# Performance work log

Hardware: AMD Instinct MI355X
Metric: run time of the kernel (lower is better)

The kernel has to match this reference:

```python
import jax, jax.numpy as jnp
import numpy as np

N, D, H = 512, 512, 1024  # n tokens, per-token dim, hidden; input_dim = 2*D


def setup_inputs() -> dict:
    key = jax.random.key(0)
    k1, k2, k3, k4, k5 = jax.random.split(key, 5)
    inp = jax.random.normal(k1, (N, D), dtype=jnp.float32)
    # torch nn.Linear stores weight [out, in]; we store transposed [in, out]
    s1 = 1.0 / np.sqrt(2 * D)
    W1 = jax.random.uniform(k2, (2 * D, H), dtype=jnp.float32, minval=-s1, maxval=s1)
    b1 = jax.random.uniform(k3, (H,), dtype=jnp.float32, minval=-s1, maxval=s1)
    s2 = 1.0 / np.sqrt(H)
    W2 = jax.random.uniform(k4, (H, 1), dtype=jnp.float32, minval=-s2, maxval=s2)
    b2 = jax.random.uniform(k5, (1,), dtype=jnp.float32, minval=-s2, maxval=s2)
    return {"input": inp, "W1": W1, "b1": b1, "W2": W2, "b2": b2}


def reference(input, W1, b1, W2, b2):
    x = jnp.squeeze(input)                       # [n, d]
    d = x.shape[1]
    # cat(x[i], x[j]) @ W1 == x[i] @ W1[:d] + x[j] @ W1[d:]
    hi = x @ W1[:d]                              # [n, h]
    hj = x @ W1[d:]                              # [n, h]
    h = jnp.tanh(hi[:, None, :] + hj[None, :, :] + b1)  # [n, n, h]
    scores = h @ W2 + b2                         # [n, n, 1]
    return scores[..., 0]                        # [n, n]
```

## Files before the change

### kernel.cpp

```cpp
#include <hip/hip_runtime.h>
#include <math.h>

#define NN 512
#define DD 512
#define HH 1024
#define C2LOG2E 2.8853900817779268f

typedef __attribute__((ext_vector_type(8))) short bf16x8;
typedef __attribute__((ext_vector_type(4))) float f32x4;

static __device__ __forceinline__ float rcp_fast(float x) {
    return __builtin_amdgcn_rcpf(x);
}
static __device__ __forceinline__ float exp2_fast(float x) {
    return __builtin_amdgcn_exp2f(x);
}
static __device__ __forceinline__ ushort f2bf(float f) {
    unsigned u = __float_as_uint(f);
    u += 0x7FFF + ((u >> 16) & 1);
    return (ushort)(u >> 16);
}
static __device__ __forceinline__ float bf2f(short u) {
    return __uint_as_float(((unsigned)(ushort)u) << 16);
}

__global__ __launch_bounds__(256) void k_convert(const float* __restrict__ x,
                                                 const float* __restrict__ W1,
                                                 const float* __restrict__ b2,
                                                 short* __restrict__ xbs,
                                                 short* __restrict__ Bts,
                                                 float* __restrict__ out) {
    __shared__ float ts[64][65];
    const int t = threadIdx.x;
    const int bx = blockIdx.x;
    if (bx < 128) {
        const int q = bx * 256 + t;
        const int g = q >> 10, ktc = (q >> 6) & 15, l = q & 63;
        const int i = g * 16 + (l & 15);
        const int k0 = ktc * 32 + (l >> 4) * 8;
        const float4 v0 = *(const float4*)&x[i * DD + k0];
        const float4 v1 = *(const float4*)&x[i * DD + k0 + 4];
        bf16x8 o;
        o[0] = (short)f2bf(v0.x); o[1] = (short)f2bf(v0.y);
        o[2] = (short)f2bf(v0.z); o[3] = (short)f2bf(v0.w);
        o[4] = (short)f2bf(v1.x); o[5] = (short)f2bf(v1.y);
        o[6] = (short)f2bf(v1.z); o[7] = (short)f2bf(v1.w);
        *(bf16x8*)&xbs[q * 8] = o;
        return;
    }
    if (bx >= 384) {
        const int f4 = (bx - 384) * 256 + t;
        const float b = b2[0];
        float4 o; o.x = b; o.y = b; o.z = b; o.w = b;
        ((float4*)out)[f4] = o;
        return;
    }
    const int tid = bx - 128;
    const int k0 = (tid >> 5) * 64;
    const int nglob = (tid & 31) * 64;
    const int off = (nglob >= 1024) ? 512 : 0;
    const int nm = nglob & 1023;
#pragma unroll
    for (int u = 0; u < 4; ++u) {
        const int f4 = t + u * 256;
        const int r = f4 >> 4, c = (f4 & 15) * 4;
        *(float4*)&ts[r][c] = *(const float4*)&W1[(off + k0 + r) * HH + nm + c];
    }
    __syncthreads();
#pragma unroll
    for (int u = 0; u < 2; ++u) {
        const int q = u * 256 + t;
        const int lg = q >> 7, lc = (q >> 6) & 1, l = q & 63;
        const int n_loc = lg * 16 + (l & 15);
        const int k_loc = lc * 32 + (l >> 4) * 8;
        bf16x8 o;
#pragma unroll
        for (int j = 0; j < 8; ++j) o[j] = (short)f2bf(ts[k_loc + j][n_loc]);
        const int gg = (nglob >> 4) + lg;
        const int ktc = (k0 >> 5) + lc;
        *(bf16x8*)&Bts[((gg * 16 + ktc) * 64 + l) * 8] = o;
    }
}

__global__ __launch_bounds__(256) void k_gemm_mfma(const short* __restrict__ xbs,
                                                   const short* __restrict__ Bts,
                                                   const float* __restrict__ b1,
                                                   short* __restrict__ Ebf) {
    const int t = threadIdx.x;
    const int w = t >> 6, l = t & 63;
    const int gi = blockIdx.x * 4 + w;
    const int by = blockIdx.y;
    const int gn0 = by * 2;

    f32x4 acc[2] = {};
    const short* ap  = xbs + gi * 8192 + l * 8;
    const short* bp0 = Bts + (gn0 + 0) * 8192 + l * 8;
    const short* bp1 = Bts + (gn0 + 1) * 8192 + l * 8;
#pragma unroll
    for (int ktc = 0; ktc < 16; ++ktc) {
        const bf16x8 a = *(const bf16x8*)(ap + ktc * 512);
        acc[0] = __builtin_amdgcn_mfma_f32_16x16x32_bf16(a, *(const bf16x8*)(bp0 + ktc * 512), acc[0], 0, 0, 0);
        acc[1] = __builtin_amdgcn_mfma_f32_16x16x32_bf16(a, *(const bf16x8*)(bp1 + ktc * 512), acc[1], 0, 0, 0);
    }
    const int lm = l & 15;
    const int orow = gi * 16 + (l >> 4) * 4;
    const bool second = (by >= 32);
#pragma unroll
    for (int c = 0; c < 2; ++c) {
        const int n = by * 32 + c * 16 + lm;
        const float badd = second ? b1[n - HH] : 0.0f;
#pragma unroll
        for (int r = 0; r < 4; ++r) {
            Ebf[(orow + r) * (2 * HH) + n] =
                (short)f2bf(exp2_fast(C2LOG2E * (acc[c][r] + badd)));
        }
    }
}

__global__ __launch_bounds__(256) void k_score(const short* __restrict__ Ebf,
                                               const float* __restrict__ W2,
                                               float* __restrict__ out) {
    __shared__ short e1s[64][72];
    __shared__ short e2s[32][72];
    __shared__ float w2s[64];
    const int t = threadIdx.x;
    const int i0 = blockIdx.x * 64, j0 = blockIdx.y * 32;
    const int hb = blockIdx.z * 64;
    const int tx = t & 15, ty = t >> 4;

#pragma unroll
    for (int u = 0; u < 2; ++u) {
        const int q = u * 256 + t;
        const int r = q >> 3, c8 = (q & 7) * 8;
        *(bf16x8*)&e1s[r][c8] = *(const bf16x8*)&Ebf[(i0 + r) * (2 * HH) + hb + c8];
    }
    {
        const int r = t >> 3, c8 = (t & 7) * 8;
        *(bf16x8*)&e2s[r][c8] = *(const bf16x8*)&Ebf[(j0 + r) * (2 * HH) + HH + hb + c8];
    }
    if (t < 64) w2s[t] = W2[hb + t];
    __syncthreads();

    float acc[4][2] = {};
    float sw = 0.0f;
    const int ty4 = ty * 4;
#pragma unroll 2
    for (int s = 0; s < 8; ++s) {
        const int h8 = s * 8;
        float ef[4][8], ff[2][8];
#pragma unroll
        for (int m = 0; m < 4; ++m) {
            const bf16x8 v = *(const bf16x8*)&e1s[ty4 + m][h8];
#pragma unroll
            for (int j = 0; j < 8; ++j) ef[m][j] = bf2f(v[j]);
        }
#pragma unroll
        for (int n = 0; n < 2; ++n) {
            const bf16x8 v = *(const bf16x8*)&e2s[tx + n * 16][h8];
#pragma unroll
            for (int j = 0; j < 8; ++j) ff[n][j] = bf2f(v[j]);
        }
        const float4 wl = *(const float4*)&w2s[h8];
        const float4 wh = *(const float4*)&w2s[h8 + 4];
#pragma unroll
        for (int m = 0; m < 4; ++m) {
#pragma unroll
            for (int n = 0; n < 2; ++n) {
                const float* em = ef[m];
                const float* fn = ff[n];
                const float d0 = __builtin_fmaf(em[0], fn[0], 1.0f);
                const float d1 = __builtin_fmaf(em[1], fn[1], 1.0f);
                const float d2 = __builtin_fmaf(em[2], fn[2], 1.0f);
                const float d3 = __builtin_fmaf(em[3], fn[3], 1.0f);
                const float d4 = __builtin_fmaf(em[4], fn[4], 1.0f);
                const float d5 = __builtin_fmaf(em[5], fn[5], 1.0f);
                const float d6 = __builtin_fmaf(em[6], fn[6], 1.0f);
                const float d7 = __builtin_fmaf(em[7], fn[7], 1.0f);
                const float d01 = d0 * d1, d23 = d2 * d3;
                const float d45 = d4 * d5, d67 = d6 * d7;
                const float n01 = __builtin_fmaf(wl.x, d1, wl.y * d0);
                const float n23 = __builtin_fmaf(wl.z, d3, wl.w * d2);
                const float n45 = __builtin_fmaf(wh.x, d5, wh.y * d4);
                const float n67 = __builtin_fmaf(wh.z, d7, wh.w * d6);
                const float N1 = __builtin_fmaf(n01, d23, n23 * d01);
                const float N2 = __builtin_fmaf(n45, d67, n67 * d45);
                const float D1 = d01 * d23, D2 = d45 * d67;
                const float Nn = __builtin_fmaf(N1, D2, N2 * D1);
                const float Dd = D1 * D2;
                acc[m][n] = __builtin_fmaf(Nn, rcp_fast(Dd), acc[m][n]);
            }
        }
        sw += wl.x + wl.y + wl.z + wl.w + wh.x + wh.y + wh.z + wh.w;
    }

#pragma unroll
    for (int m = 0; m < 4; ++m) {
        const int row = i0 + ty4 + m;
#pragma unroll
        for (int n = 0; n < 2; ++n) {
            const int col = j0 + tx + n * 16;
            atomicAdd(&out[row * NN + col], sw - 2.0f * acc[m][n]);
        }
    }
}

extern "C" void kernel_launch(void* const* d_in, const int* in_sizes, int n_in,
                              void* d_out, int out_size, void* d_ws, size_t ws_size,
                              hipStream_t stream) {
    const float* x  = (const float*)d_in[0];
    const float* W1 = (const float*)d_in[1];
    const float* b1 = (const float*)d_in[2];
    const float* W2 = (const float*)d_in[3];
    const float* b2 = (const float*)d_in[4];
    float* out = (float*)d_out;

    short* Ebf = (short*)d_ws;
    short* xbs = Ebf + NN * 2 * HH;
    short* Bts = xbs + NN * DD;

    k_convert<<<dim3(640), 256, 0, stream>>>(x, W1, b2, xbs, Bts, out);
    k_gemm_mfma<<<dim3(8, 64), 256, 0, stream>>>(xbs, Bts, b1, Ebf);
    k_score<<<dim3(8, 16, 16), 256, 0, stream>>>(Ebf, W2, out);
}
```

Baseline: 42.34 us.

## Fuse fp32-to-bf16 conversion into the MFMA GEMM and drop the convert kernel

Removes the separate conversion kernel that pre-packed x and W1 into bf16 MFMA layouts. The GEMM kernel now reads fp32 x and W1 directly, stages a 32x32 W1 tile through shared memory, and converts to bf16 on the fly before each MFMA. Output initialisation with b2 moves into extra blocks of the same kernel. This saves a launch and a round trip through global memory, but each W1 tile is now re-read and re-converted by every row block, and two barriers are added per k-step.

```diff
diff --git a/kernel.cpp b/kernel.cpp
--- a/kernel.cpp
+++ b/kernel.cpp
@@ -24,90 +24,68 @@
     return __uint_as_float(((unsigned)(ushort)u) << 16);
 }
 
-__global__ __launch_bounds__(256) void k_convert(const float* __restrict__ x,
-                                                 const float* __restrict__ W1,
-                                                 const float* __restrict__ b2,
-                                                 short* __restrict__ xbs,
-                                                 short* __restrict__ Bts,
-                                                 float* __restrict__ out) {
-    __shared__ float ts[64][65];
+__global__ __launch_bounds__(256) void k_gemm_fused(const float* __restrict__ x,
+                                                    const float* __restrict__ W1,
+                                                    const float* __restrict__ b1,
+                                                    const float* __restrict__ b2,
+                                                    short* __restrict__ Ebf,
+                                                    float* __restrict__ out) {
+    const int bx = blockIdx.x;
     const int t = threadIdx.x;
-    const int bx = blockIdx.x;
-    if (bx < 128) {
-        const int q = bx * 256 + t;
-        const int g = q >> 10, ktc = (q >> 6) & 15, l = q & 63;
-        const int i = g * 16 + (l & 15);
-        const int k0 = ktc * 32 + (l >> 4) * 8;
-        const float4 v0 = *(const float4*)&x[i * DD + k0];
-        const float4 v1 = *(const float4*)&x[i * DD + k0 + 4];
-        bf16x8 o;
-        o[0] = (short)f2bf(v0.x); o[1] = (short)f2bf(v0.y);
-        o[2] = (short)f2bf(v0.z); o[3] = (short)f2bf(v0.w);
-        o[4] = (short)f2bf(v1.x); o[5] = (short)f2bf(v1.y);
-        o[6] = (short)f2bf(v1.z); o[7] = (short)f2bf(v1.w);
-        *(bf16x8*)&xbs[q * 8] = o;
-        return;
-    }
-    if (bx >= 384) {
-        const int f4 = (bx - 384) * 256 + t;
+    if (bx >= 512) {
+        const int f4 = (bx - 512) * 256 + t;
         const float b = b2[0];
         float4 o; o.x = b; o.y = b; o.z = b; o.w = b;
         ((float4*)out)[f4] = o;
         return;
     }
-    const int tid = bx - 128;
-    const int k0 = (tid >> 5) * 64;
-    const int nglob = (tid & 31) * 64;
-    const int off = (nglob >= 1024) ? 512 : 0;
-    const int nm = nglob & 1023;
-#pragma unroll
-    for (int u = 0; u < 4; ++u) {
-        const int f4 = t + u * 256;
-        const int r = f4 >> 4, c = (f4 & 15) * 4;
-        *(float4*)&ts[r][c] = *(const float4*)&W1[(off + k0 + r) * HH + nm + c];
-    }
-    __syncthreads();
-#pragma unroll
-    for (int u = 0; u < 2; ++u) {
-        const int q = u * 256 + t;
-        const int lg = q >> 7, lc = (q >> 6) & 1, l = q & 63;
-        const int n_loc = lg * 16 + (l & 15);
-        const int k_loc = lc * 32 + (l >> 4) * 8;
-        bf16x8 o;
-#pragma unroll
-        for (int j = 0; j < 8; ++j) o[j] = (short)f2bf(ts[k_loc + j][n_loc]);
-        const int gg = (nglob >> 4) + lg;
-        const int ktc = (k0 >> 5) + lc;
-        *(bf16x8*)&Bts[((gg * 16 + ktc) * 64 + l) * 8] = o;
-    }
-}
+    __shared__ float ws[32][33];
+    const int w = t >> 6, l = t & 63;
+    const int bi = bx >> 6;
+    const int bn = bx & 63;
+    const int i0 = bi * 64;
+    const int nglob = bn * 32;
+    const int koff = (nglob >= HH) ? DD : 0;
+    const int nc0 = nglob & (HH - 1);
+    const int nl = l & 15;
+    const int kr8 = (l >> 4) * 8;
+    const int skrow = t >> 3;
+    const int sc4 = (t & 7) * 4;
 
-__global__ __launch_bounds__(256) void k_gemm_mfma(const short* __restrict__ xbs,
-                                                   const short* __restrict__ Bts,
-                                                   const float* __restrict__ b1,
-                                                   short* __restrict__ Ebf) {
-    const int t = threadIdx.x;
-    const int w = t >> 6, l = t & 63;
-    const int gi = blockIdx.x * 4 + w;
-    const int by = blockIdx.y;
-    const int gn0 = by * 2;
+    const float* xp = x + (i0 + w * 16 + nl) * DD + kr8;
+    const float* wp = W1 + (koff + skrow) * HH + nc0 + sc4;
 
     f32x4 acc[2] = {};
-    const short* ap  = xbs + gi * 8192 + l * 8;
-    const short* bp0 = Bts + (gn0 + 0) * 8192 + l * 8;
-    const short* bp1 = Bts + (gn0 + 1) * 8192 + l * 8;
+#pragma unroll 2
+    for (int kc = 0; kc < 16; ++kc) {
+        const float4 wv = *(const float4*)(wp + kc * 32 * HH);
+        const float4 a0 = *(const float4*)(xp + kc * 32);
+        const float4 a1 = *(const float4*)(xp + kc * 32 + 4);
+        __syncthreads();
+        ws[skrow][sc4 + 0] = wv.x;
+        ws[skrow][sc4 + 1] = wv.y;
+        ws[skrow][sc4 + 2] = wv.z;
+        ws[skrow][sc4 + 3] = wv.w;
+        bf16x8 af;
+        af[0] = (short)f2bf(a0.x); af[1] = (short)f2bf(a0.y);
+        af[2] = (short)f2bf(a0.z); af[3] = (short)f2bf(a0.w);
+        af[4] = (short)f2bf(a1.x); af[5] = (short)f2bf(a1.y);
+        af[6] = (short)f2bf(a1.z); af[7] = (short)f2bf(a1.w);
+        __syncthreads();
 #pragma unroll
-    for (int ktc = 0; ktc < 16; ++ktc) {
-        const bf16x8 a = *(const bf16x8*)(ap + ktc * 512);
-        acc[0] = __builtin_amdgcn_mfma_f32_16x16x32_bf16(a, *(const bf16x8*)(bp0 + ktc * 512), acc[0], 0, 0, 0);
-        acc[1] = __builtin_amdgcn_mfma_f32_16x16x32_bf16(a, *(const bf16x8*)(bp1 + ktc * 512), acc[1], 0, 0, 0);
+        for (int c = 0; c < 2; ++c) {
+            bf16x8 bf;
+#pragma unroll
+            for (int j = 0; j < 8; ++j)
+                bf[j] = (short)f2bf(ws[kr8 + j][c * 16 + nl]);
+            acc[c] = __builtin_amdgcn_mfma_f32_16x16x32_bf16(af, bf, acc[c], 0, 0, 0);
+        }
     }
-    const int lm = l & 15;
-    const int orow = gi * 16 + (l >> 4) * 4;
-    const bool second = (by >= 32);
+    const int orow = i0 + w * 16 + (l >> 4) * 4;
+    const bool second = (nglob >= HH);
 #pragma unroll
     for (int c = 0; c < 2; ++c) {
-        const int n = by * 32 + c * 16 + lm;
+        const int n = nglob + c * 16 + nl;
         const float badd = second ? b1[n - HH] : 0.0f;
 #pragma unroll
         for (int r = 0; r < 4; ++r) {
@@ -215,10 +193,7 @@
     float* out = (float*)d_out;
 
     short* Ebf = (short*)d_ws;
-    short* xbs = Ebf + NN * 2 * HH;
-    short* Bts = xbs + NN * DD;
 
-    k_convert<<<dim3(640), 256, 0, stream>>>(x, W1, b2, xbs, Bts, out);
-    k_gemm_mfma<<<dim3(8, 64), 256, 0, stream>>>(xbs, Bts, b1, Ebf);
+    k_gemm_fused<<<dim3(768), 256, 0, stream>>>(x, W1, b1, b2, Ebf, out);
     k_score<<<dim3(8, 16, 16), 256, 0, stream>>>(Ebf, W2, out);
 }
```

Measured after the change: 43.21 us. 2.1% more time.
